# Optimization experiments

Hardware: AMD Instinct MI355X
Metric: run time of the kernel (lower is better)

Reference implementation:

```python
import jax, jax.numpy as jnp
import numpy as np

NUM_ITERATIONS = 3
EPS = 1e-08

def squash(s, axis=-1):
    norm = jnp.linalg.norm(s, axis=axis, keepdims=True)
    scale = norm ** 2 / (1 + norm ** 2)
    return scale * s / (norm + EPS)

def setup_inputs() -> dict:
    key = jax.random.key(0)
    k1, k2 = jax.random.split(key)
    B, C, M, O, I = 256, 1152, 8, 16, 8
    u = jax.random.normal(k1, (B, C, I), dtype=jnp.float32)
    W = jax.random.normal(k2, (C, M, O, I), dtype=jnp.float32)
    return {"u": u, "W": W}

def reference(u, W):
    B, C, I = u.shape
    M, O = W.shape[1], W.shape[2]
    # u_hat: [B, C, M, O] -- predicted output capsule vectors
    u_hat = jnp.einsum('cmoi,bci->bcmo', W, u)
    b = jnp.zeros((B, C, M), dtype=u.dtype)
    v = None
    for r in range(NUM_ITERATIONS):
        c = jax.nn.softmax(b, axis=2)  # softmax over emotion dim
        s = jnp.einsum('bcm,bcmo->bmo', c, u_hat)
        v = squash(s)  # [B, M, O]
        if r < NUM_ITERATIONS - 1:
            uv = jnp.einsum('bcmo,bmo->bcm', u_hat, v)
            b = b + uv
    return v
```

## Files before the change

### kernel.cpp

```cpp
#include <hip/hip_runtime.h>

#define B_SZ 256
#define C_SZ 1152
#define MO   128
#define CAPS_EPS 1e-8f

#define CSPL 32
#define CRNG (C_SZ / CSPL)
#define BPB  8
#define CPW  (CRNG / 4)

struct alignas(8) H4 { _Float16 h[4]; };
union PK2 { unsigned int u32; _Float16 h[2]; };

__global__ __launch_bounds__(256) void caps_uhat_p0(
    const float* __restrict__ u,
    const float* __restrict__ W,
    unsigned int* __restrict__ uhat,
    float* __restrict__ part0)
{
    const int bid = blockIdx.x;
    const int csp = bid >> 5;
    const int bt  = bid & 31;
    const int c0  = csp * CRNG;
    const int b0  = bt * BPB;
    const int tid = threadIdx.x;
    const int l   = tid & 63;
    const int wv  = tid >> 6;

    __shared__ __align__(16) float u_sh[BPB][292];
    __shared__ __align__(16) float s_lds[4][BPB][MO];

    for (int idx = tid; idx < BPB * 72; idx += 256) {
        const int bb = idx / 72, off = idx % 72;
        *reinterpret_cast<float4*>(&u_sh[bb][off * 4]) =
            *reinterpret_cast<const float4*>(
                u + ((size_t)(b0 + bb) * C_SZ + c0) * 8 + off * 4);
    }
    __syncthreads();

    float acc[BPB][2];
#pragma unroll
    for (int bb = 0; bb < BPB; ++bb) { acc[bb][0] = 0.f; acc[bb][1] = 0.f; }

    for (int k = 0; k < CPW; ++k) {
        const int cl = wv * CPW + k;
        const int c  = c0 + cl;
        const float4* wp =
            reinterpret_cast<const float4*>(W + (size_t)c * 1024) + l * 4;
        const float4 wa = wp[0], wb = wp[1], wc4 = wp[2], wd = wp[3];
        unsigned int* ub = uhat + ((size_t)c * B_SZ + b0) * 64 + l;
        const int cb = cl * 8;
#pragma unroll
        for (int bb = 0; bb < BPB; ++bb) {
            const float4 u0 = *reinterpret_cast<const float4*>(&u_sh[bb][cb]);
            const float4 u1 =
                *reinterpret_cast<const float4*>(&u_sh[bb][cb + 4]);
            float h0 = wa.x*u0.x + wa.y*u0.y + wa.z*u0.z + wa.w*u0.w
                     + wb.x*u1.x + wb.y*u1.y + wb.z*u1.z + wb.w*u1.w;
            float h1 = wc4.x*u0.x + wc4.y*u0.y + wc4.z*u0.z + wc4.w*u0.w
                     + wd.x*u1.x + wd.y*u1.y + wd.z*u1.z + wd.w*u1.w;
            PK2 pk;
            pk.h[0] = (_Float16)h0;
            pk.h[1] = (_Float16)h1;
            ub[(size_t)bb * 64] = pk.u32;
            acc[bb][0] += h0;
            acc[bb][1] += h1;
        }
    }

#pragma unroll
    for (int bb = 0; bb < BPB; ++bb)
        *reinterpret_cast<float2*>(&s_lds[wv][bb][2 * l]) =
            make_float2(acc[bb][0] * 0.125f, acc[bb][1] * 0.125f);
    __syncthreads();

    {
        const int bb = tid >> 5, j = tid & 31;
        float4 r = make_float4(0.f, 0.f, 0.f, 0.f);
#pragma unroll
        for (int w = 0; w < 4; ++w) {
            const float4 x =
                *reinterpret_cast<const float4*>(&s_lds[w][bb][4 * j]);
            r.x += x.x; r.y += x.y; r.z += x.z; r.w += x.w;
        }
        *reinterpret_cast<float4*>(
            part0 + ((size_t)csp * B_SZ + b0 + bb) * MO + 4 * j) = r;
    }
}

template <int PASS>
__global__ __launch_bounds__(256) void caps_route_f(
    const float* __restrict__ part_in,
    float* __restrict__ v0_io,
    const H4* __restrict__ uhat,
    float* __restrict__ part_out)
{
    const int bid = blockIdx.x;
    const int csp = bid >> 5;
    const int bt  = bid & 31;
    const int c0  = csp * CRNG;
    const int b0  = bt * BPB;
    const int tid = threadIdx.x;

    __shared__ __align__(16) float v_sh[BPB][MO];

    {
        const int bb = tid >> 5, j = tid & 31;
        float4 s = make_float4(0.f, 0.f, 0.f, 0.f);
        for (int k = 0; k < CSPL; ++k) {
            const float4 x = *reinterpret_cast<const float4*>(
                part_in + ((size_t)k * B_SZ + b0 + bb) * MO + 4 * j);
            s.x += x.x; s.y += x.y; s.z += x.z; s.w += x.w;
        }
        float n2 = s.x*s.x + s.y*s.y + s.z*s.z + s.w*s.w;
        n2 += __shfl_xor(n2, 1);
        n2 += __shfl_xor(n2, 2);
        const float norm = sqrtf(n2);
        const float sc = (n2 / (1.f + n2)) / (norm + CAPS_EPS);
        float4 v = make_float4(s.x * sc, s.y * sc, s.z * sc, s.w * sc);
        if (PASS == 1) {
            if (csp == 0)
                *reinterpret_cast<float4*>(
                    v0_io + (size_t)(b0 + bb) * MO + 4 * j) = v;
        } else {
            const float4 p = *reinterpret_cast<const float4*>(
                v0_io + (size_t)(b0 + bb) * MO + 4 * j);
            v.x += p.x; v.y += p.y; v.z += p.z; v.w += p.w;
        }
        *reinterpret_cast<float4*>(&v_sh[bb][4 * j]) = v;
    }
    __syncthreads();

    const int g = tid >> 5;
    const int l = tid & 31;
    const int b = b0 + g;
    const float4 v4 = *reinterpret_cast<const float4*>(&v_sh[g][4 * l]);
    float acc[4] = {0.f, 0.f, 0.f, 0.f};

    const H4* base = uhat + ((size_t)c0 * B_SZ + b) * 32 + l;

    H4 r0 = base[0];
    H4 r1 = base[(size_t)B_SZ * 32];

    for (int cl = 0; cl < CRNG; cl += 2) {
        H4 n0 = r0, n1 = r1;
        if (cl + 2 < CRNG) {
            n0 = base[(size_t)(cl + 2) * B_SZ * 32];
            n1 = base[(size_t)(cl + 3) * B_SZ * 32];
        }
#pragma unroll
        for (int q = 0; q < 2; ++q) {
            const H4 r = q ? r1 : r0;
            const float uh0 = (float)r.h[0], uh1 = (float)r.h[1];
            const float uh2 = (float)r.h[2], uh3 = (float)r.h[3];
            float uv = uh0 * v4.x + uh1 * v4.y + uh2 * v4.z + uh3 * v4.w;
            uv += __shfl_xor(uv, 1);
            uv += __shfl_xor(uv, 2);
            float mx = fmaxf(uv, __shfl_xor(uv, 4));
            mx = fmaxf(mx, __shfl_xor(mx, 8));
            mx = fmaxf(mx, __shfl_xor(mx, 16));
            const float e = expf(uv - mx);
            float den = e;
            den += __shfl_xor(den, 4);
            den += __shfl_xor(den, 8);
            den += __shfl_xor(den, 16);
            const float cw = e / den;
            acc[0] = fmaf(cw, uh0, acc[0]);
            acc[1] = fmaf(cw, uh1, acc[1]);
            acc[2] = fmaf(cw, uh2, acc[2]);
            acc[3] = fmaf(cw, uh3, acc[3]);
        }
        r0 = n0; r1 = n1;
    }
    *reinterpret_cast<float4*>(
        part_out + ((size_t)csp * B_SZ + b) * MO + 4 * l) =
        make_float4(acc[0], acc[1], acc[2], acc[3]);
}

__global__ __launch_bounds__(128) void caps_vcalc(
    const float* __restrict__ part_in,
    float* __restrict__ vout,
    int nsplit)
{
    const int b = blockIdx.x, t = threadIdx.x;
    float s = 0.f;
    for (int k = 0; k < nsplit; ++k)
        s += part_in[((size_t)k * B_SZ + b) * MO + t];
    float n2 = s * s;
    n2 += __shfl_xor(n2, 1);
    n2 += __shfl_xor(n2, 2);
    n2 += __shfl_xor(n2, 4);
    n2 += __shfl_xor(n2, 8);
    const float norm = sqrtf(n2);
    vout[(size_t)b * MO + t] = (n2 / (1.f + n2)) * s / (norm + CAPS_EPS);
}

template <int R>
__global__ __launch_bounds__(256) void caps_small(
    const float* __restrict__ u, const float* __restrict__ W,
    const float* __restrict__ s_in, const float* __restrict__ v0_in,
    float* __restrict__ s_out, float* __restrict__ v0_out,
    float* __restrict__ out)
{
    const int b = blockIdx.x, tid = threadIdx.x;
    __shared__ float sh_v[8][17];
    __shared__ float sh_part[256][17];

    if (R >= 1) {
        if (tid < 128) {
            float val = s_in[b * 128 + tid];
            float n2 = val * val;
            n2 += __shfl_xor(n2, 1); n2 += __shfl_xor(n2, 2);
            n2 += __shfl_xor(n2, 4); n2 += __shfl_xor(n2, 8);
            float norm = sqrtf(n2);
            float v = (n2 / (1.f + n2)) * val / (norm + CAPS_EPS);
            int m = tid >> 4, o = tid & 15;
            if (R == 1) { v0_out[b * 128 + tid] = v; sh_v[m][o] = v; }
            else        { sh_v[m][o] = v + v0_in[b * 128 + tid]; }
        }
        __syncthreads();
    }
    const int c_local = tid >> 3, m = tid & 7;
    float s_acc[16];
#pragma unroll
    for (int o = 0; o < 16; ++o) s_acc[o] = 0.f;
    for (int cc = 0; cc < C_SZ; cc += 32) {
        const int c = cc + c_local;
        const float4* up = reinterpret_cast<const float4*>(
            u + (size_t)(b * C_SZ + c) * 8);
        float4 u0 = up[0], u1 = up[1];
        float u8[8] = {u0.x, u0.y, u0.z, u0.w, u1.x, u1.y, u1.z, u1.w};
        float uh[16];
        const float4* wp = reinterpret_cast<const float4*>(
            W + (size_t)((c * 8 + m) * 16) * 8);
#pragma unroll
        for (int o = 0; o < 16; ++o) {
            float4 w0 = wp[o * 2], w1 = wp[o * 2 + 1];
            uh[o] = w0.x * u8[0] + w0.y * u8[1] + w0.z * u8[2] + w0.w * u8[3] +
                    w1.x * u8[4] + w1.y * u8[5] + w1.z * u8[6] + w1.w * u8[7];
        }
        float cw;
        if (R == 0) cw = 0.125f;
        else {
            float uv = 0.f;
#pragma unroll
            for (int o = 0; o < 16; ++o) uv = fmaf(uh[o], sh_v[m][o], uv);
            float mx = uv;
            mx = fmaxf(mx, __shfl_xor(mx, 1));
            mx = fmaxf(mx, __shfl_xor(mx, 2));
            mx = fmaxf(mx, __shfl_xor(mx, 4));
            float e = expf(uv - mx);
            float den = e;
            den += __shfl_xor(den, 1); den += __shfl_xor(den, 2);
            den += __shfl_xor(den, 4);
            cw = e / den;
        }
#pragma unroll
        for (int o = 0; o < 16; ++o) s_acc[o] = fmaf(cw, uh[o], s_acc[o]);
    }
#pragma unroll
    for (int o = 0; o < 16; ++o) sh_part[tid][o] = s_acc[o];
    __syncthreads();
    if (tid < 128) {
        const int m2 = tid >> 4, o2 = tid & 15;
        float s = 0.f;
#pragma unroll
        for (int gg = 0; gg < 32; ++gg) s += sh_part[gg * 8 + m2][o2];
        if (R < 2) s_out[b * 128 + tid] = s;
        else {
            float n2 = s * s;
            n2 += __shfl_xor(n2, 1); n2 += __shfl_xor(n2, 2);
            n2 += __shfl_xor(n2, 4); n2 += __shfl_xor(n2, 8);
            float norm = sqrtf(n2);
            out[b * 128 + tid] = (n2 / (1.f + n2)) * s / (norm + CAPS_EPS);
        }
    }
}

extern "C" void kernel_launch(void* const* d_in, const int* in_sizes, int n_in,
                              void* d_out, int out_size, void* d_ws, size_t ws_size,
                              hipStream_t stream) {
    const float* u = (const float*)d_in[0];
    const float* W = (const float*)d_in[1];
    float* out = (float*)d_out;

    const size_t UHAT_BYTES = (size_t)C_SZ * B_SZ * MO * 2;
    const size_t PR_FLOATS  = (size_t)CSPL * B_SZ * MO;
    const size_t NEED = UHAT_BYTES + (2 * PR_FLOATS + B_SZ * MO) * 4;

    if (ws_size >= NEED) {
        unsigned int* uhat_w = (unsigned int*)d_ws;
        const H4* uhat_r = (const H4*)d_ws;
        float* part0 = (float*)((char*)d_ws + UHAT_BYTES);
        float* partA = part0 + PR_FLOATS;
        float* v0    = partA + PR_FLOATS;

        dim3 blk(256), grid(CSPL * 32);
        caps_uhat_p0 <<<grid, blk, 0, stream>>>(u, W, uhat_w, part0);
        caps_route_f<1><<<grid, blk, 0, stream>>>(part0, v0, uhat_r, partA);
        caps_route_f<2><<<grid, blk, 0, stream>>>(partA, v0, uhat_r, part0);
        caps_vcalc<<<dim3(B_SZ), dim3(128), 0, stream>>>(part0, out, CSPL);
    } else {
        float* sA = (float*)d_ws;
        float* sB = sA + 32768;
        float* v0 = sB + 32768;
        dim3 grid(B_SZ), blk(256);
        caps_small<0><<<grid, blk, 0, stream>>>(u, W, nullptr, nullptr, sA, nullptr, nullptr);
        caps_small<1><<<grid, blk, 0, stream>>>(u, W, sA, nullptr, sB, v0, nullptr);
        caps_small<2><<<grid, blk, 0, stream>>>(u, W, sB, v0, nullptr, nullptr, out);
    }
}
```

Measured before the change: 80.24 us.

## Recompute u_hat from W and u in each routing pass instead of storing fp16

Drops the materialised fp16 u_hat buffer (about 75 MB) that the first kernel wrote and both routing passes read back. Each routing pass now reloads u into shared memory and recomputes u_hat on the fly from W, then does the dot product with v, the softmax over the 8 output capsules using 64-lane shuffles, and the weighted accumulation. A cross-wave LDS reduction produces the partial sums. This trades heavy global memory traffic for repeated FMA work and also removes the fp16 rounding of u_hat.

```diff
diff --git a/kernel.cpp b/kernel.cpp
--- a/kernel.cpp
+++ b/kernel.cpp
@@ -10,23 +10,16 @@
 #define BPB  8
 #define CPW  (CRNG / 4)
 
-struct alignas(8) H4 { _Float16 h[4]; };
-union PK2 { unsigned int u32; _Float16 h[2]; };
-
-__global__ __launch_bounds__(256) void caps_uhat_p0(
+
+__global__ __launch_bounds__(256) void caps_pass0(
     const float* __restrict__ u,
     const float* __restrict__ W,
-    unsigned int* __restrict__ uhat,
     float* __restrict__ part0)
 {
     const int bid = blockIdx.x;
-    const int csp = bid >> 5;
-    const int bt  = bid & 31;
-    const int c0  = csp * CRNG;
-    const int b0  = bt * BPB;
-    const int tid = threadIdx.x;
-    const int l   = tid & 63;
-    const int wv  = tid >> 6;
+    const int csp = bid >> 5, bt = bid & 31;
+    const int c0 = csp * CRNG, b0 = bt * BPB;
+    const int tid = threadIdx.x, l = tid & 63, wv = tid >> 6;
 
     __shared__ __align__(16) float u_sh[BPB][292];
     __shared__ __align__(16) float s_lds[4][BPB][MO];
@@ -45,27 +38,19 @@
 
     for (int k = 0; k < CPW; ++k) {
         const int cl = wv * CPW + k;
-        const int c  = c0 + cl;
-        const float4* wp =
-            reinterpret_cast<const float4*>(W + (size_t)c * 1024) + l * 4;
+        const float4* wp = reinterpret_cast<const float4*>(
+            W + (size_t)(c0 + cl) * 1024) + l * 4;
         const float4 wa = wp[0], wb = wp[1], wc4 = wp[2], wd = wp[3];
-        unsigned int* ub = uhat + ((size_t)c * B_SZ + b0) * 64 + l;
         const int cb = cl * 8;
 #pragma unroll
         for (int bb = 0; bb < BPB; ++bb) {
             const float4 u0 = *reinterpret_cast<const float4*>(&u_sh[bb][cb]);
             const float4 u1 =
                 *reinterpret_cast<const float4*>(&u_sh[bb][cb + 4]);
-            float h0 = wa.x*u0.x + wa.y*u0.y + wa.z*u0.z + wa.w*u0.w
-                     + wb.x*u1.x + wb.y*u1.y + wb.z*u1.z + wb.w*u1.w;
-            float h1 = wc4.x*u0.x + wc4.y*u0.y + wc4.z*u0.z + wc4.w*u0.w
-                     + wd.x*u1.x + wd.y*u1.y + wd.z*u1.z + wd.w*u1.w;
-            PK2 pk;
-            pk.h[0] = (_Float16)h0;
-            pk.h[1] = (_Float16)h1;
-            ub[(size_t)bb * 64] = pk.u32;
-            acc[bb][0] += h0;
-            acc[bb][1] += h1;
+            acc[bb][0] += wa.x*u0.x + wa.y*u0.y + wa.z*u0.z + wa.w*u0.w
+                        + wb.x*u1.x + wb.y*u1.y + wb.z*u1.z + wb.w*u1.w;
+            acc[bb][1] += wc4.x*u0.x + wc4.y*u0.y + wc4.z*u0.z + wc4.w*u0.w
+                        + wd.x*u1.x + wd.y*u1.y + wd.z*u1.z + wd.w*u1.w;
         }
     }
 
@@ -90,20 +75,28 @@
 }
 
 template <int PASS>
-__global__ __launch_bounds__(256) void caps_route_f(
+__global__ __launch_bounds__(256) void caps_pass12(
     const float* __restrict__ part_in,
     float* __restrict__ v0_io,
-    const H4* __restrict__ uhat,
+    const float* __restrict__ u,
+    const float* __restrict__ W,
     float* __restrict__ part_out)
 {
     const int bid = blockIdx.x;
-    const int csp = bid >> 5;
-    const int bt  = bid & 31;
-    const int c0  = csp * CRNG;
-    const int b0  = bt * BPB;
-    const int tid = threadIdx.x;
-
+    const int csp = bid >> 5, bt = bid & 31;
+    const int c0 = csp * CRNG, b0 = bt * BPB;
+    const int tid = threadIdx.x, l = tid & 63, wv = tid >> 6;
+
+    __shared__ __align__(16) float u_sh[BPB][292];
     __shared__ __align__(16) float v_sh[BPB][MO];
+    __shared__ __align__(16) float s_lds[4][BPB][MO];
+
+    for (int idx = tid; idx < BPB * 72; idx += 256) {
+        const int bb = idx / 72, off = idx % 72;
+        *reinterpret_cast<float4*>(&u_sh[bb][off * 4]) =
+            *reinterpret_cast<const float4*>(
+                u + ((size_t)(b0 + bb) * C_SZ + c0) * 8 + off * 4);
+    }
 
     {
         const int bb = tid >> 5, j = tid & 31;
@@ -132,50 +125,65 @@
     }
     __syncthreads();
 
-    const int g = tid >> 5;
-    const int l = tid & 31;
-    const int b = b0 + g;
-    const float4 v4 = *reinterpret_cast<const float4*>(&v_sh[g][4 * l]);
-    float acc[4] = {0.f, 0.f, 0.f, 0.f};
-
-    const H4* base = uhat + ((size_t)c0 * B_SZ + b) * 32 + l;
-
-    H4 r0 = base[0];
-    H4 r1 = base[(size_t)B_SZ * 32];
-
-    for (int cl = 0; cl < CRNG; cl += 2) {
-        H4 n0 = r0, n1 = r1;
-        if (cl + 2 < CRNG) {
-            n0 = base[(size_t)(cl + 2) * B_SZ * 32];
-            n1 = base[(size_t)(cl + 3) * B_SZ * 32];
-        }
-#pragma unroll
-        for (int q = 0; q < 2; ++q) {
-            const H4 r = q ? r1 : r0;
-            const float uh0 = (float)r.h[0], uh1 = (float)r.h[1];
-            const float uh2 = (float)r.h[2], uh3 = (float)r.h[3];
-            float uv = uh0 * v4.x + uh1 * v4.y + uh2 * v4.z + uh3 * v4.w;
+    float acc[BPB][2];
+#pragma unroll
+    for (int bb = 0; bb < BPB; ++bb) { acc[bb][0] = 0.f; acc[bb][1] = 0.f; }
+
+    for (int k = 0; k < CPW; ++k) {
+        const int cl = wv * CPW + k;
+        const float4* wp = reinterpret_cast<const float4*>(
+            W + (size_t)(c0 + cl) * 1024) + l * 4;
+        const float4 wa = wp[0], wb = wp[1], wc4 = wp[2], wd = wp[3];
+        const int cb = cl * 8;
+#pragma unroll
+        for (int bb = 0; bb < BPB; ++bb) {
+            const float4 u0 = *reinterpret_cast<const float4*>(&u_sh[bb][cb]);
+            const float4 u1 =
+                *reinterpret_cast<const float4*>(&u_sh[bb][cb + 4]);
+            const float h0 =
+                  wa.x*u0.x + wa.y*u0.y + wa.z*u0.z + wa.w*u0.w
+                + wb.x*u1.x + wb.y*u1.y + wb.z*u1.z + wb.w*u1.w;
+            const float h1 =
+                  wc4.x*u0.x + wc4.y*u0.y + wc4.z*u0.z + wc4.w*u0.w
+                + wd.x*u1.x + wd.y*u1.y + wd.z*u1.z + wd.w*u1.w;
+
+            const float2 vv =
+                *reinterpret_cast<const float2*>(&v_sh[bb][2 * l]);
+            float uv = h0 * vv.x + h1 * vv.y;
             uv += __shfl_xor(uv, 1);
             uv += __shfl_xor(uv, 2);
-            float mx = fmaxf(uv, __shfl_xor(uv, 4));
-            mx = fmaxf(mx, __shfl_xor(mx, 8));
+            uv += __shfl_xor(uv, 4);
+            float mx = fmaxf(uv, __shfl_xor(uv, 8));
             mx = fmaxf(mx, __shfl_xor(mx, 16));
+            mx = fmaxf(mx, __shfl_xor(mx, 32));
             const float e = expf(uv - mx);
-            float den = e;
-            den += __shfl_xor(den, 4);
-            den += __shfl_xor(den, 8);
+            float den = e + __shfl_xor(e, 8);
             den += __shfl_xor(den, 16);
+            den += __shfl_xor(den, 32);
             const float cw = e / den;
-            acc[0] = fmaf(cw, uh0, acc[0]);
-            acc[1] = fmaf(cw, uh1, acc[1]);
-            acc[2] = fmaf(cw, uh2, acc[2]);
-            acc[3] = fmaf(cw, uh3, acc[3]);
-        }
-        r0 = n0; r1 = n1;
-    }
-    *reinterpret_cast<float4*>(
-        part_out + ((size_t)csp * B_SZ + b) * MO + 4 * l) =
-        make_float4(acc[0], acc[1], acc[2], acc[3]);
+            acc[bb][0] = fmaf(cw, h0, acc[bb][0]);
+            acc[bb][1] = fmaf(cw, h1, acc[bb][1]);
+        }
+    }
+
+#pragma unroll
+    for (int bb = 0; bb < BPB; ++bb)
+        *reinterpret_cast<float2*>(&s_lds[wv][bb][2 * l]) =
+            make_float2(acc[bb][0], acc[bb][1]);
+    __syncthreads();
+
+    {
+        const int bb = tid >> 5, j = tid & 31;
+        float4 r = make_float4(0.f, 0.f, 0.f, 0.f);
+#pragma unroll
+        for (int w = 0; w < 4; ++w) {
+            const float4 x =
+                *reinterpret_cast<const float4*>(&s_lds[w][bb][4 * j]);
+            r.x += x.x; r.y += x.y; r.z += x.z; r.w += x.w;
+        }
+        *reinterpret_cast<float4*>(
+            part_out + ((size_t)csp * B_SZ + b0 + bb) * MO + 4 * j) = r;
+    }
 }
 
 __global__ __launch_bounds__(128) void caps_vcalc(
@@ -285,21 +293,18 @@
     const float* W = (const float*)d_in[1];
     float* out = (float*)d_out;
 
-    const size_t UHAT_BYTES = (size_t)C_SZ * B_SZ * MO * 2;
-    const size_t PR_FLOATS  = (size_t)CSPL * B_SZ * MO;
-    const size_t NEED = UHAT_BYTES + (2 * PR_FLOATS + B_SZ * MO) * 4;
+    const size_t PR_FLOATS = (size_t)CSPL * B_SZ * MO;
+    const size_t NEED = (2 * PR_FLOATS + B_SZ * MO) * 4;
 
     if (ws_size >= NEED) {
-        unsigned int* uhat_w = (unsigned int*)d_ws;
-        const H4* uhat_r = (const H4*)d_ws;
-        float* part0 = (float*)((char*)d_ws + UHAT_BYTES);
+        float* part0 = (float*)d_ws;
         float* partA = part0 + PR_FLOATS;
         float* v0    = partA + PR_FLOATS;
 
         dim3 blk(256), grid(CSPL * 32);
-        caps_uhat_p0 <<<grid, blk, 0, stream>>>(u, W, uhat_w, part0);
-        caps_route_f<1><<<grid, blk, 0, stream>>>(part0, v0, uhat_r, partA);
-        caps_route_f<2><<<grid, blk, 0, stream>>>(partA, v0, uhat_r, part0);
+        caps_pass0    <<<grid, blk, 0, stream>>>(u, W, part0);
+        caps_pass12<1><<<grid, blk, 0, stream>>>(part0, v0, u, W, partA);
+        caps_pass12<2><<<grid, blk, 0, stream>>>(partA, v0, u, W, part0);
         caps_vcalc<<<dim3(B_SZ), dim3(128), 0, stream>>>(part0, out, CSPL);
     } else {
         float* sA = (float*)d_ws;
```

Result: slower. 117.1 us (+46.0%).
